# Kernel tuning notes

Hardware: AMD Instinct MI355X
Metric: run time of the kernel (lower is better)

The kernel has to match this reference:

```python
import jax, jax.numpy as jnp
import numpy as np

WORLD_SIZE = 8
M = 4096
N = 4096
K_LOCAL = 1024  # full K = WORLD_SIZE * K_LOCAL = 8192


def setup_inputs() -> dict:
    key = jax.random.key(0)
    k1, k2 = jax.random.split(key)
    # Per-rank activation shard [R, M, K_local] and weight shard [R, N, K_local]
    inp = jax.random.normal(k1, (WORLD_SIZE, M, K_LOCAL), dtype=jnp.float32) * 0.02
    w = jax.random.normal(k2, (WORLD_SIZE, N, K_LOCAL), dtype=jnp.float32) * 0.02
    return {"input": inp, "weight": w}


def reference(input, weight):
    # Each rank r computes a partial GEMM: input[r] @ weight[r].T -> [M, N].
    # Reduce(-scatter) sums partials over ranks; the single einsum contracts
    # both the rank axis (the all-reduce part) and K_local (the GEMM part).
    full = jnp.einsum("rmk,rnk->mn", input, weight)  # [M, N]
    R = input.shape[0]
    # Scatter: rank r receives rows [r*M/R : (r+1)*M/R] -> stacked [R, M/R, N]
    return full.reshape(R, full.shape[0] // R, full.shape[1])
```

## Files before the change

### kernel.cpp

```cpp
#include <hip/hip_runtime.h>
#include <cstdint>
#include <cstddef>


#define M_DIM 4096
#define N_DIM 4096
#define K_DIM 8192
#define K_LOCAL 1024
#define RANKS 8
#define NT 128

typedef __bf16 bf16x8 __attribute__((ext_vector_type(8)));
typedef float f32x4 __attribute__((ext_vector_type(4)));

__device__ __forceinline__ unsigned short f2bf(float f) {
    unsigned int u = __float_as_uint(f);
    unsigned int r = (u + 0x7fffu + ((u >> 16) & 1u)) >> 16;
    return (unsigned short)r;
}

__global__ __launch_bounds__(256) void convert_cast(
    const float* __restrict__ srcA, unsigned short* __restrict__ dstA,
    const float* __restrict__ srcB, unsigned short* __restrict__ dstB,
    int blocks_per_tensor) {
    const float* src = srcA;
    unsigned short* dst = dstA;
    int b = blockIdx.x;
    if (b >= blocks_per_tensor) { b -= blocks_per_tensor; src = srcB; dst = dstB; }
    size_t base = (size_t)b * 4096 + threadIdx.x * 4;
#pragma unroll
    for (int i = 0; i < 4; ++i) {
        size_t e = base + i * 1024;
        f32x4 v = __builtin_nontemporal_load((const f32x4*)(src + e));
        ushort4 o;
        o.x = f2bf(v.x); o.y = f2bf(v.y); o.z = f2bf(v.z); o.w = f2bf(v.w);
        *(ushort4*)(dst + e) = o;
    }
}

__device__ __forceinline__ void gll16(const unsigned short* g, unsigned short* l) {
    __builtin_amdgcn_global_load_lds(
        (const __attribute__((address_space(1))) void*)g,
        (__attribute__((address_space(3))) void*)l,
        16, 0, 0);
}

__device__ __forceinline__ int k_off(int t) {
    return ((t >> 4) << 22) | ((t & 15) << 6);
}

#define VM4 asm volatile("s_waitcnt vmcnt(4)" ::: "memory")
#define VM0 asm volatile("s_waitcnt vmcnt(0)" ::: "memory")
#define VMNONE ((void)0)
#define LGKM0 asm volatile("s_waitcnt lgkmcnt(0)" ::: "memory")

#define STAGE_A(TOFF, HALF, PBUF) { \
    _Pragma("unroll") for (int j_ = 0; j_ < 2; ++j_) \
        gll16(A + (size_t)((TOFF) + (HALF) * 131072 + thrA[j_]), \
              smem + (PBUF) * 16384 + (HALF) * 8192 + ldsOff[j_]); }

#define STAGE_B(TOFF, HALF, PBUF) { \
    _Pragma("unroll") for (int j_ = 0; j_ < 2; ++j_) \
        gll16(B + (size_t)((TOFF) + (HALF) * 131072 + thrB[j_]), \
              smem + 32768 + (PBUF) * 16384 + (HALF) * 8192 + ldsOff[j_]); }

#define READ_A(DST, BASE, MOFF) { \
    _Pragma("unroll") for (int ks_ = 0; ks_ < 2; ++ks_) \
        _Pragma("unroll") for (int mm_ = 0; mm_ < 4; ++mm_) \
            DST[ks_][mm_] = *(const bf16x8*)&(BASE)[(((MOFF) + mm_) * 16 + l15) * 64 + (ks_ ? swz1 : swz0)]; }

#define READ_B(DST, BASE, NJ0) { \
    _Pragma("unroll") for (int ks_ = 0; ks_ < 2; ++ks_) \
        _Pragma("unroll") for (int nn_ = 0; nn_ < 2; ++nn_) \
            DST[ks_][nn_] = *(const bf16x8*)&(BASE)[(bRowBase + ((NJ0) + nn_) * 16 + l15) * 64 + (ks_ ? swz1 : swz0)]; }

#define QUAD(AF, BF, MI0, NJ0) { \
    __builtin_amdgcn_s_setprio(1); \
    _Pragma("unroll") for (int ks_ = 0; ks_ < 2; ++ks_) \
        _Pragma("unroll") for (int mm_ = 0; mm_ < 4; ++mm_) \
            _Pragma("unroll") for (int nn_ = 0; nn_ < 2; ++nn_) \
                acc[(MI0) + mm_][(NJ0) + nn_] = __builtin_amdgcn_mfma_f32_16x16x32_bf16( \
                    AF[ks_][mm_], BF[ks_][nn_], acc[(MI0) + mm_][(NJ0) + nn_], 0, 0, 0); \
    __builtin_amdgcn_s_setprio(0); }

#define KTILE(PBUF, KT, SB, SA, VMOP) { \
    const int t1off_ = k_off((KT) + 1); \
    const int t2off_ = k_off((KT) + 2); \
    unsigned short* aC_ = smem + (PBUF) * 16384 + wmIdx * 8192; \
    unsigned short* bC_ = smem + 32768 + (PBUF) * 16384 + bHalfSel * 8192; \
     \
    READ_A(aLo, aC_, 0) \
    READ_B(bLoF, bC_, 0) \
    if (SB) { STAGE_B(t1off_, 0, (PBUF) ^ 1) } \
    __builtin_amdgcn_s_barrier(); \
    LGKM0; \
    QUAD(aLo, bLoF, 0, 0) \
    __builtin_amdgcn_s_barrier(); \
     \
    READ_A(aHi, aC_, 4) \
    if (SB) { STAGE_B(t1off_, 1, (PBUF) ^ 1) } \
    __builtin_amdgcn_s_barrier(); \
    LGKM0; \
    QUAD(aHi, bLoF, 4, 0) \
    __builtin_amdgcn_s_barrier(); \
     \
    READ_B(bHiF, bC_, 2) \
    if (SA) { STAGE_A(t2off_, 0, (PBUF)) } \
    __builtin_amdgcn_s_barrier(); \
    LGKM0; \
    QUAD(aLo, bHiF, 0, 2) \
    __builtin_amdgcn_s_barrier(); \
     \
    if (SA) { STAGE_A(t2off_, 1, (PBUF)) } \
    __builtin_amdgcn_s_barrier(); \
    LGKM0; \
    QUAD(aHi, bHiF, 4, 2) \
    VMOP; \
    __builtin_amdgcn_s_barrier(); \
}

__global__ __launch_bounds__(512, 2) void gemm_bf16_8ph(
    const unsigned short* __restrict__ A,
    const unsigned short* __restrict__ B,
    float* __restrict__ C) {
    extern __shared__ unsigned short smem[];

    const int tid = threadIdx.x;
    const int lane = tid & 63;
    const int wave = tid >> 6;
    const int wmIdx = wave >> 2;
    const int wn = wave & 3;
    const int l15 = lane & 15;
    const int l4 = lane >> 4;
    const int bHalfSel = wn >> 1;
    const int bRowBase = (wn & 1) * 64;

    const int bid = blockIdx.x;
    const int xcd = bid & 7;
    const int idx = bid >> 3;
    const int tm = (xcd >> 2) * 8 + (idx >> 2);
    const int tn = (xcd & 3) * 4 + (idx & 3);
    const int bm0 = tm * 256;
    const int bn0 = tn * 256;

    int thrA[2], thrB[2], ldsOff[2];
#pragma unroll
    for (int j = 0; j < 2; ++j) {
        int cc = j * 512 + tid;
        int row = cc >> 3;
        int col = ((cc & 7) ^ (row & 7)) * 8;
        thrA[j] = (bm0 + row) * K_LOCAL + col;
        thrB[j] = (bn0 + row) * K_LOCAL + col;
        ldsOff[j] = cc * 8;
    }

    const int swz0 = ((0 + l4) ^ (l15 & 7)) * 8;
    const int swz1 = ((4 + l4) ^ (l15 & 7)) * 8;

    bf16x8 aLo[2][4], aHi[2][4], bLoF[2][2], bHiF[2][2];
    f32x4 acc[8][4] = {};

    STAGE_A(0, 0, 0)
    STAGE_A(0, 1, 0)
    STAGE_B(0, 0, 0)
    STAGE_B(0, 1, 0)
    STAGE_A(64, 0, 1)
    STAGE_A(64, 1, 1)
    VM4;
    __builtin_amdgcn_s_barrier();

#pragma unroll 1
    for (int kt = 0; kt < 126; kt += 2) {
        KTILE(0, kt, 1, 1, VM4)
        KTILE(1, kt + 1, 1, 1, VM4)
    }
    KTILE(0, 126, 1, 0, VM0)
    KTILE(1, 127, 0, 0, VMNONE)

#pragma unroll
    for (int mi = 0; mi < 8; ++mi) {
        int row0 = bm0 + wmIdx * 128 + mi * 16 + l4 * 4;
#pragma unroll
        for (int nj = 0; nj < 4; ++nj) {
            int col = bn0 + wn * 64 + nj * 16 + l15;
#pragma unroll
            for (int r = 0; r < 4; ++r)
                C[(size_t)(row0 + r) * N_DIM + col] = acc[mi][nj][r];
        }
    }
}

__global__ __launch_bounds__(256) void gemm_bf16_128(
    const unsigned short* __restrict__ A,
    const unsigned short* __restrict__ B,
    float* __restrict__ C) {
    __shared__ __align__(16) unsigned short As[128 * 64];
    __shared__ __align__(16) unsigned short Bs[128 * 64];

    const int tid = threadIdx.x;
    const int lane = tid & 63;
    const int wave = tid >> 6;
    const int wm = (wave >> 1) * 64;
    const int wnn = (wave & 1) * 64;
    const int l15 = lane & 15;
    const int l4 = lane >> 4;

    const int bid = blockIdx.x;
    const int xcd = bid & 7;
    const int q = bid >> 3;
    const int st = (q >> 2) * 8 + xcd;
    const int pos = q & 3;
    const int bm0 = ((st >> 4) * 2 + (pos >> 1)) * 128;
    const int bn0 = ((st & 15) * 2 + (pos & 1)) * 128;

    const unsigned short* ga[4];
    const unsigned short* gb[4];
    int lo[4];
#pragma unroll
    for (int p = 0; p < 4; ++p) {
        int cc = p * 256 + tid;
        int row = cc >> 3;
        int cpos = cc & 7;
        int col = (cpos ^ (row & 7)) * 8;
        ga[p] = A + (size_t)(bm0 + row) * K_LOCAL + col;
        gb[p] = B + (size_t)(bn0 + row) * K_LOCAL + col;
        lo[p] = cc * 8;
    }

    const int swz0 = ((l4 + 0) ^ (l15 & 7)) * 8;
    const int swz1 = ((l4 + 4) ^ (l15 & 7)) * 8;
    const int a_row = (wm + l15) * 64;
    const int b_row = (wnn + l15) * 64;

    f32x4 acc[4][4] = {};

    for (int r = 0; r < RANKS; ++r) {
        const size_t roff = (size_t)r * (M_DIM * (size_t)K_LOCAL);
        for (int kl = 0; kl < K_LOCAL; kl += 64) {
#pragma unroll
            for (int p = 0; p < 4; ++p) {
                gll16(ga[p] + roff + kl, &As[lo[p]]);
                gll16(gb[p] + roff + kl, &Bs[lo[p]]);
            }
            __syncthreads();
#pragma unroll
            for (int ks = 0; ks < 2; ++ks) {
                const int swz = ks ? swz1 : swz0;
                bf16x8 af[4], bfr[4];
#pragma unroll
                for (int i = 0; i < 4; ++i)
                    af[i] = *(const bf16x8*)&As[a_row + i * 16 * 64 + swz];
#pragma unroll
                for (int j = 0; j < 4; ++j)
                    bfr[j] = *(const bf16x8*)&Bs[b_row + j * 16 * 64 + swz];
#pragma unroll
                for (int i = 0; i < 4; ++i)
#pragma unroll
                    for (int j = 0; j < 4; ++j)
                        acc[i][j] = __builtin_amdgcn_mfma_f32_16x16x32_bf16(
                            af[i], bfr[j], acc[i][j], 0, 0, 0);
            }
            __syncthreads();
        }
    }

#pragma unroll
    for (int i = 0; i < 4; ++i) {
        int row0 = bm0 + wm + i * 16 + l4 * 4;
#pragma unroll
        for (int j = 0; j < 4; ++j) {
            int col = bn0 + wnn + j * 16 + l15;
#pragma unroll
            for (int r = 0; r < 4; ++r)
                C[(size_t)(row0 + r) * N_DIM + col] = acc[i][j][r];
        }
    }
}

__global__ void gemm_naive(const float* __restrict__ A, const float* __restrict__ B,
                           float* __restrict__ C) {
    __shared__ float As[16][17];
    __shared__ float Bs[16][17];
    int tx = threadIdx.x, ty = threadIdx.y;
    int m = blockIdx.y * 16 + ty;
    int n0 = blockIdx.x * 16;
    float accv = 0.f;
    for (int kt = 0; kt < K_DIM; kt += 16) {
        int r = kt >> 10;
        int k = (kt & 1023) + tx;
        As[ty][tx] = A[((size_t)r * M_DIM + m) * K_LOCAL + k];
        Bs[ty][tx] = B[((size_t)r * N_DIM + (n0 + ty)) * K_LOCAL + k];
        __syncthreads();
#pragma unroll
        for (int kk = 0; kk < 16; ++kk) accv += As[ty][kk] * Bs[tx][kk];
        __syncthreads();
    }
    C[(size_t)m * N_DIM + n0 + tx] = accv;
}

extern "C" void kernel_launch(void* const* d_in, const int* in_sizes, int n_in,
                              void* d_out, int out_size, void* d_ws, size_t ws_size,
                              hipStream_t stream) {
    const float* inp = (const float*)d_in[0];
    const float* wgt = (const float*)d_in[1];
    float* out = (float*)d_out;

    const size_t elems = (size_t)M_DIM * K_DIM;
    const size_t need = 2 * elems * sizeof(unsigned short);

    if (ws_size >= need) {
        unsigned short* Abf = (unsigned short*)d_ws;
        unsigned short* Bbf = Abf + elems;
        const int bpt = (int)(elems / 4096);
        convert_cast<<<bpt * 2, 256, 0, stream>>>(inp, Abf, wgt, Bbf, bpt);

        static int dynOK = -1;
        if (dynOK < 0) {
            dynOK = (hipFuncSetAttribute((const void*)gemm_bf16_8ph,
                                         hipFuncAttributeMaxDynamicSharedMemorySize,
                                         131072) == hipSuccess)
                        ? 1
                        : 0;
        }
        if (dynOK) {
            gemm_bf16_8ph<<<256, 512, 131072, stream>>>(Abf, Bbf, out);
        } else {
            gemm_bf16_128<<<1024, 256, 0, stream>>>(Abf, Bbf, out);
        }
    } else {
        dim3 grid(N_DIM / 16, M_DIM / 16);
        dim3 block(16, 16);
        gemm_naive<<<grid, block, 0, stream>>>(inp, wgt, out);
    }
}
```

Measured before the change: 275.5 us.

## Switch GEMM to 32x32x16 MFMA tiles and stage B-half earlier

Replaces the 16x16x32 bf16 MFMA inner product with 32x32x16 MFMA, rewriting the LDS fragment reads, swizzle indexing, accumulator layout and epilogue store mapping. It also reorders the global-to-LDS staging so half of the next B tile is prefetched one phase earlier, with deeper vmcnt waits and a partial lgkmcnt wait. Larger MFMA tiles aim to cut LDS read traffic and instruction count per FLOP. The reordered staging touches the buffer currently being read, which risks hazards and changes register pressure.

```diff
diff --git a/kernel.cpp b/kernel.cpp
--- a/kernel.cpp
+++ b/kernel.cpp
@@ -8,10 +8,10 @@
 #define K_DIM 8192
 #define K_LOCAL 1024
 #define RANKS 8
-#define NT 128
 
 typedef __bf16 bf16x8 __attribute__((ext_vector_type(8)));
 typedef float f32x4 __attribute__((ext_vector_type(4)));
+typedef float f32x16 __attribute__((ext_vector_type(16)));
 
 __device__ __forceinline__ unsigned short f2bf(float f) {
     unsigned int u = __float_as_uint(f);
@@ -49,10 +49,11 @@
     return ((t >> 4) << 22) | ((t & 15) << 6);
 }
 
-#define VM4 asm volatile("s_waitcnt vmcnt(4)" ::: "memory")
+#define VM6 asm volatile("s_waitcnt vmcnt(6)" ::: "memory")
 #define VM0 asm volatile("s_waitcnt vmcnt(0)" ::: "memory")
 #define VMNONE ((void)0)
 #define LGKM0 asm volatile("s_waitcnt lgkmcnt(0)" ::: "memory")
+#define LGKM8 asm volatile("s_waitcnt lgkmcnt(8)" ::: "memory")
 
 #define STAGE_A(TOFF, HALF, PBUF) { \
     _Pragma("unroll") for (int j_ = 0; j_ < 2; ++j_) \
@@ -64,57 +65,58 @@
         gll16(B + (size_t)((TOFF) + (HALF) * 131072 + thrB[j_]), \
               smem + 32768 + (PBUF) * 16384 + (HALF) * 8192 + ldsOff[j_]); }
 
-#define READ_A(DST, BASE, MOFF) { \
-    _Pragma("unroll") for (int ks_ = 0; ks_ < 2; ++ks_) \
-        _Pragma("unroll") for (int mm_ = 0; mm_ < 4; ++mm_) \
-            DST[ks_][mm_] = *(const bf16x8*)&(BASE)[(((MOFF) + mm_) * 16 + l15) * 64 + (ks_ ? swz1 : swz0)]; }
-
-#define READ_B(DST, BASE, NJ0) { \
-    _Pragma("unroll") for (int ks_ = 0; ks_ < 2; ++ks_) \
-        _Pragma("unroll") for (int nn_ = 0; nn_ < 2; ++nn_) \
-            DST[ks_][nn_] = *(const bf16x8*)&(BASE)[(bRowBase + ((NJ0) + nn_) * 16 + l15) * 64 + (ks_ ? swz1 : swz0)]; }
-
-#define QUAD(AF, BF, MI0, NJ0) { \
+#define READ_A32(DST, BASE, AM0) { \
+    _Pragma("unroll") for (int ks_ = 0; ks_ < 4; ++ks_) \
+        _Pragma("unroll") for (int am_ = 0; am_ < 2; ++am_) \
+            DST[ks_][am_] = *(const bf16x8*)&(BASE)[ \
+                (((AM0) + am_) * 32 + l31) * 64 + ((ks_ * 2 + lhi) ^ (l31 & 7)) * 8]; }
+
+#define READ_B32(DST, BASE, BN) { \
+    _Pragma("unroll") for (int ks_ = 0; ks_ < 4; ++ks_) \
+        DST[ks_] = *(const bf16x8*)&(BASE)[ \
+            (bRowBase + (BN) * 32 + l31) * 64 + ((ks_ * 2 + lhi) ^ (l31 & 7)) * 8]; }
+
+#define QUAD32(AF, BF_, AM0, BN) { \
     __builtin_amdgcn_s_setprio(1); \
-    _Pragma("unroll") for (int ks_ = 0; ks_ < 2; ++ks_) \
-        _Pragma("unroll") for (int mm_ = 0; mm_ < 4; ++mm_) \
-            _Pragma("unroll") for (int nn_ = 0; nn_ < 2; ++nn_) \
-                acc[(MI0) + mm_][(NJ0) + nn_] = __builtin_amdgcn_mfma_f32_16x16x32_bf16( \
-                    AF[ks_][mm_], BF[ks_][nn_], acc[(MI0) + mm_][(NJ0) + nn_], 0, 0, 0); \
+    _Pragma("unroll") for (int ks_ = 0; ks_ < 4; ++ks_) \
+        _Pragma("unroll") for (int am_ = 0; am_ < 2; ++am_) \
+            acc[(AM0) + am_][BN] = __builtin_amdgcn_mfma_f32_32x32x16_bf16( \
+                AF[ks_][am_], BF_[ks_], acc[(AM0) + am_][BN], 0, 0, 0); \
     __builtin_amdgcn_s_setprio(0); }
 
-#define KTILE(PBUF, KT, SB, SA, VMOP) { \
+#define KTILE32(PBUF, KT, SB1, SA, SB0, VMOP) { \
     const int t1off_ = k_off((KT) + 1); \
     const int t2off_ = k_off((KT) + 2); \
     unsigned short* aC_ = smem + (PBUF) * 16384 + wmIdx * 8192; \
     unsigned short* bC_ = smem + 32768 + (PBUF) * 16384 + bHalfSel * 8192; \
      \
-    READ_A(aLo, aC_, 0) \
-    READ_B(bLoF, bC_, 0) \
-    if (SB) { STAGE_B(t1off_, 0, (PBUF) ^ 1) } \
+    READ_A32(aLo, aC_, 0) \
+    READ_B32(bLoF, bC_, 0) \
+    if (SB1) { STAGE_B(t1off_, 1, (PBUF) ^ 1) } \
+    LGKM8; \
     __builtin_amdgcn_s_barrier(); \
     LGKM0; \
-    QUAD(aLo, bLoF, 0, 0) \
+    QUAD32(aLo, bLoF, 0, 0) \
     __builtin_amdgcn_s_barrier(); \
      \
-    READ_A(aHi, aC_, 4) \
-    if (SB) { STAGE_B(t1off_, 1, (PBUF) ^ 1) } \
+    READ_A32(aHi, aC_, 2) \
+    if (SA) { STAGE_A(t2off_, 0, (PBUF)) } \
     __builtin_amdgcn_s_barrier(); \
     LGKM0; \
-    QUAD(aHi, bLoF, 4, 0) \
+    QUAD32(aHi, bLoF, 2, 0) \
     __builtin_amdgcn_s_barrier(); \
      \
-    READ_B(bHiF, bC_, 2) \
-    if (SA) { STAGE_A(t2off_, 0, (PBUF)) } \
+    READ_B32(bHiF, bC_, 1) \
+    if (SA) { STAGE_A(t2off_, 1, (PBUF)) } \
     __builtin_amdgcn_s_barrier(); \
     LGKM0; \
-    QUAD(aLo, bHiF, 0, 2) \
+    QUAD32(aLo, bHiF, 0, 1) \
     __builtin_amdgcn_s_barrier(); \
      \
-    if (SA) { STAGE_A(t2off_, 1, (PBUF)) } \
+    if (SB0) { STAGE_B(t2off_, 0, (PBUF)) } \
     __builtin_amdgcn_s_barrier(); \
     LGKM0; \
-    QUAD(aHi, bHiF, 4, 2) \
+    QUAD32(aHi, bHiF, 2, 1) \
     VMOP; \
     __builtin_amdgcn_s_barrier(); \
 }
@@ -130,8 +132,8 @@
     const int wave = tid >> 6;
     const int wmIdx = wave >> 2;
     const int wn = wave & 3;
-    const int l15 = lane & 15;
-    const int l4 = lane >> 4;
+    const int l31 = lane & 31;
+    const int lhi = lane >> 5;
     const int bHalfSel = wn >> 1;
     const int bRowBase = (wn & 1) * 64;
 
@@ -154,11 +156,8 @@
         ldsOff[j] = cc * 8;
     }
 
-    const int swz0 = ((0 + l4) ^ (l15 & 7)) * 8;
-    const int swz1 = ((4 + l4) ^ (l15 & 7)) * 8;
-
-    bf16x8 aLo[2][4], aHi[2][4], bLoF[2][2], bHiF[2][2];
-    f32x4 acc[8][4] = {};
+    bf16x8 aLo[4][2], aHi[4][2], bLoF[4], bHiF[4];
+    f32x16 acc[4][2] = {};
 
     STAGE_A(0, 0, 0)
     STAGE_A(0, 1, 0)
@@ -166,26 +165,28 @@
     STAGE_B(0, 1, 0)
     STAGE_A(64, 0, 1)
     STAGE_A(64, 1, 1)
-    VM4;
+    STAGE_B(64, 0, 1)
+    VM6;
     __builtin_amdgcn_s_barrier();
 
 #pragma unroll 1
     for (int kt = 0; kt < 126; kt += 2) {
-        KTILE(0, kt, 1, 1, VM4)
-        KTILE(1, kt + 1, 1, 1, VM4)
-    }
-    KTILE(0, 126, 1, 0, VM0)
-    KTILE(1, 127, 0, 0, VMNONE)
-
-#pragma unroll
-    for (int mi = 0; mi < 8; ++mi) {
-        int row0 = bm0 + wmIdx * 128 + mi * 16 + l4 * 4;
-#pragma unroll
-        for (int nj = 0; nj < 4; ++nj) {
-            int col = bn0 + wn * 64 + nj * 16 + l15;
-#pragma unroll
-            for (int r = 0; r < 4; ++r)
-                C[(size_t)(row0 + r) * N_DIM + col] = acc[mi][nj][r];
+        KTILE32(0, kt, 1, 1, 1, VM6)
+        KTILE32(1, kt + 1, 1, 1, 1, VM6)
+    }
+    KTILE32(0, 126, 1, 0, 0, VM0)
+    KTILE32(1, 127, 0, 0, 0, VMNONE)
+
+#pragma unroll
+    for (int am = 0; am < 4; ++am) {
+#pragma unroll
+        for (int bn = 0; bn < 2; ++bn) {
+            int col = bn0 + wn * 64 + bn * 32 + l31;
+#pragma unroll
+            for (int reg = 0; reg < 16; ++reg) {
+                int row = bm0 + wmIdx * 128 + am * 32 + (reg & 3) + 8 * (reg >> 2) + 4 * lhi;
+                C[(size_t)row * N_DIM + col] = acc[am][bn][reg];
+            }
         }
     }
 }
```

After: 314.8 us. +14.3%, slower.
